# Kernel tuning notes

Measured on AMD Instinct MI355X. Metric: run time of the kernel, lower is better.

Reference implementation:

```python
import jax, jax.numpy as jnp
import numpy as np

TEMPERATURE = 0.1
SIGMA = 1.0
NUM_CLASSES = 4
INF = 1e8
EPS = 1e-12


def _l2_normalize(x):
    n = jnp.sqrt(jnp.sum(x * x, axis=-1, keepdims=True))
    return x / jnp.maximum(n, EPS)


def _rbf_kernel(y, gamma):
    # y: [M, P] -> [M, M] exp(-gamma * ||yi - yj||^2)
    sq = jnp.sum(y * y, axis=-1)
    d2 = sq[:, None] + sq[None, :] - 2.0 * (y @ y.T)
    d2 = jnp.maximum(d2, 0.0)
    return jnp.exp(-gamma * d2)


def setup_inputs() -> dict:
    key = jax.random.key(0)
    k1, k2, k3, k4 = jax.random.split(key, 4)
    N, D = 2048, 512
    return {
        "z_i": jax.random.normal(k1, (N, D), dtype=jnp.float32),
        "z_j": jax.random.normal(k2, (N, D), dtype=jnp.float32),
        "labels": jax.random.randint(k3, (N,), 0, NUM_CLASSES, dtype=jnp.int64),
        "z_pos": jax.random.uniform(k4, (N, 1), dtype=jnp.float32),
    }


def reference(z_i, z_j, labels, z_pos):
    N = z_i.shape[0]
    zi = _l2_normalize(z_i)
    zj = _l2_normalize(z_j)

    eye_n = jnp.eye(N, dtype=zi.dtype)
    sim_zii = (zi @ zi.T) / TEMPERATURE - INF * eye_n
    sim_zjj = (zj @ zj.T) / TEMPERATURE - INF * eye_n
    sim_zij = (zi @ zj.T) / TEMPERATURE

    # label agreement mask over the 2N x 2N augmented batch
    labs = jax.nn.one_hot(labels, NUM_CLASSES, dtype=jnp.float32)
    L = jnp.concatenate([labs, labs], axis=0)          # [2N, C]
    eye_2n = jnp.eye(2 * N, dtype=jnp.float32)
    mask = (L @ L.T) * (1.0 - eye_2n)

    # RBF kernel weights over positional labels (detached in original)
    all_pos = jnp.tile(z_pos.reshape(N, -1), (2, 1))   # [2N, P]
    gamma = 1.0 / (2.0 * SIGMA ** 2)
    weights = _rbf_kernel(all_pos, gamma) * (1.0 - eye_2n)

    final_weights = weights * mask
    # NB: torch broadcasting divides column j by rowsum[j]; matrix is symmetric
    final_weights = final_weights / final_weights.sum(axis=1)

    top = jnp.concatenate([sim_zii, sim_zij], axis=1)
    bot = jnp.concatenate([sim_zij.T, sim_zjj], axis=1)
    sim_Z = jnp.concatenate([top, bot], axis=0)        # [2N, 2N]

    log_sim_Z = jax.nn.log_softmax(sim_Z, axis=1)
    loss = (-1.0 / N) * jnp.sum(log_sim_Z * final_weights)
    return loss
```

## Files before the change

kernel.cpp:

```cpp
#include <hip/hip_runtime.h>
#include <hip/hip_bf16.h>

#define D 512
#define INV_T 10.0f
#define INF_VAL 1e8f

#define BM 128
#define BN 128
#define BK 64
#define KSTEPS (D / BK)
#define NCHUNK 64

typedef short bf16x8 __attribute__((ext_vector_type(8)));
typedef float f32x4 __attribute__((ext_vector_type(4)));

typedef __attribute__((address_space(3))) unsigned int lds_uint;
typedef __attribute__((address_space(1))) unsigned int gbl_uint;

__device__ __forceinline__ void async_copy16(const ushort* gsrc, ushort* ldst) {
  __builtin_amdgcn_global_load_lds((const gbl_uint*)gsrc, (lds_uint*)ldst, 16, 0, 0);
}

__device__ inline float wave_reduce_sum(float v) {
#pragma unroll
  for (int off = 32; off > 0; off >>= 1) v += __shfl_xor(v, off);
  return v;
}

__global__ __launch_bounds__(256) void k_normcast(const float* __restrict__ zi,
                                                  const float* __restrict__ zj,
                                                  ushort* __restrict__ zb, int N) {
  __shared__ float scratch[4];
  __shared__ float s_inv;
  int row = blockIdx.x;
  const float* src = (row < N) ? (zi + (size_t)row * D) : (zj + (size_t)(row - N) * D);
  float ss = 0.f;
  for (int k = threadIdx.x; k < D; k += 256) {
    float v = src[k];
    ss = fmaf(v, v, ss);
  }
  ss = wave_reduce_sum(ss);
  int lane = threadIdx.x & 63, wv = threadIdx.x >> 6;
  if (lane == 0) scratch[wv] = ss;
  __syncthreads();
  if (threadIdx.x == 0) {
    float t = scratch[0] + scratch[1] + scratch[2] + scratch[3];
    s_inv = 1.0f / fmaxf(sqrtf(t), 1e-12f);
  }
  __syncthreads();
  float sc = s_inv;
  ushort* dst = zb + (size_t)row * D;
  for (int k = threadIdx.x; k < D; k += 256) {
    __hip_bfloat16 h = __float2bfloat16(src[k] * sc);
    dst[k] = *reinterpret_cast<ushort*>(&h);
  }
}

__global__ __launch_bounds__(256) void k_colsum(const int* __restrict__ labels,
                                                const float* __restrict__ zpos,
                                                float* __restrict__ sinv, int N) {
  __shared__ float scratch[4];
  int j = blockIdx.x;
  int lj = labels[j];
  float pj = zpos[j];
  float s = 0.f;
  for (int i = threadIdx.x; i < N; i += 256) {
    if (labels[i] == lj) {
      float d = zpos[i] - pj;
      s += __expf(-0.5f * d * d);
    }
  }
  s = wave_reduce_sum(s);
  int lane = threadIdx.x & 63, wv = threadIdx.x >> 6;
  if (lane == 0) scratch[wv] = s;
  __syncthreads();
  if (threadIdx.x == 0) {
    float t = scratch[0] + scratch[1] + scratch[2] + scratch[3];
    sinv[j] = 1.0f / (2.0f * t - 1.0f);
  }
}

__global__ __launch_bounds__(256) void k_tt(const int* __restrict__ labels,
                                            const float* __restrict__ zpos,
                                            const float* __restrict__ sinv,
                                            float* __restrict__ tt, int N) {
  __shared__ float scratch[4];
  int i = blockIdx.x;
  int li = labels[i];
  float pi = zpos[i];
  float s = 0.f;
  for (int j = threadIdx.x; j < N; j += 256) {
    if (labels[j] == li) {
      float d = zpos[j] - pi;
      s += __expf(-0.5f * d * d) * sinv[j];
    }
  }
  s = wave_reduce_sum(s);
  int lane = threadIdx.x & 63, wv = threadIdx.x >> 6;
  if (lane == 0) scratch[wv] = s;
  __syncthreads();
  if (threadIdx.x == 0) {
    tt[i] = scratch[0] + scratch[1] + scratch[2] + scratch[3];
  }
}

__global__ __launch_bounds__(256, 4) void k_gemm(
    const ushort* __restrict__ zb, const int* __restrict__ labels,
    const float* __restrict__ zpos, const float* __restrict__ sinv,
    float* __restrict__ s_ws, float* __restrict__ c_ws, int N) {
  __shared__ __align__(16) ushort As[BM * BK];
  __shared__ __align__(16) ushort Bs[BN * BK];

  const int tid = threadIdx.x;
  const int lane = tid & 63;
  const int wv = tid >> 6;
  const int wr = wv >> 1;
  const int wc = wv & 1;
  const int colq = lane & 15;
  const int laneg = lane >> 4;

  const int bid = blockIdx.x;
  const int L = (bid & 7) * 128 + (bid >> 3);
  const int rt = L >> 5;
  const int ct = L & 31;
  const int rowBase = rt * BM;
  const int colBase = ct * BN;
  const int twoN = 2 * N;

  const int srow = lane >> 3;
  const int sslot = (lane & 7) ^ srow;

  f32x4 acc[4][4] = {};

  for (int kt = 0; kt < KSTEPS; ++kt) {
#pragma unroll
    for (int q = 0; q < 4; ++q) {
      int rloc = wv * 32 + q * 8;
      async_copy16(zb + (size_t)(rowBase + rloc + srow) * D + kt * BK + sslot * 8,
                   (ushort*)As + rloc * BK);
      async_copy16(zb + (size_t)(colBase + rloc + srow) * D + kt * BK + sslot * 8,
                   (ushort*)Bs + rloc * BK);
    }
    __syncthreads();

#pragma unroll
    for (int kk = 0; kk < 2; ++kk) {
      bf16x8 a[4], b[4];
      const int slot = (kk * 4 + laneg);
#pragma unroll
      for (int rf = 0; rf < 4; ++rf) {
        int r = wr * 64 + rf * 16 + colq;
        a[rf] = *reinterpret_cast<const bf16x8*>(
            reinterpret_cast<const char*>(As) + r * 128 + (slot ^ (r & 7)) * 16);
      }
#pragma unroll
      for (int cf = 0; cf < 4; ++cf) {
        int c = wc * 64 + cf * 16 + colq;
        b[cf] = *reinterpret_cast<const bf16x8*>(
            reinterpret_cast<const char*>(Bs) + c * 128 + (slot ^ (c & 7)) * 16);
      }
#pragma unroll
      for (int rf = 0; rf < 4; ++rf)
#pragma unroll
        for (int cf = 0; cf < 4; ++cf)
          acc[rf][cf] = __builtin_amdgcn_mfma_f32_16x16x32_bf16(a[rf], b[cf], acc[rf][cf], 0, 0, 0);
    }
    __syncthreads();
  }

  const int wRowBase = rowBase + wr * 64;
  const int wColBase = colBase + wc * 64;
  const int rmodBase = (wRowBase >= N) ? wRowBase - N : wRowBase;
  const int cmodBase = (wColBase >= N) ? wColBase - N : wColBase;

  float rpos[16];
  unsigned rlab = 0;
#pragma unroll
  for (int rf = 0; rf < 4; ++rf)
#pragma unroll
    for (int rg = 0; rg < 4; ++rg) {
      int idx = rf * 4 + rg;
      int r = rmodBase + rf * 16 + laneg * 4 + rg;
      rpos[idx] = zpos[r];
      rlab |= ((unsigned)labels[r] & 3u) << (idx * 2);
    }

  float s_p[16], c_p[16];
#pragma unroll
  for (int i = 0; i < 16; ++i) { s_p[i] = 0.f; c_p[i] = 0.f; }

#pragma unroll
  for (int cf = 0; cf < 4; ++cf) {
    int jc = cmodBase + cf * 16 + colq;
    int lc = labels[jc];
    float pc = zpos[jc];
    float si = sinv[jc];
    int col = wColBase + cf * 16 + colq;
#pragma unroll
    for (int rf = 0; rf < 4; ++rf)
#pragma unroll
      for (int rg = 0; rg < 4; ++rg) {
        int idx = rf * 4 + rg;
        int row = wRowBase + rf * 16 + laneg * 4 + rg;
        float sim = acc[rf][cf][rg] * INV_T;
        bool diag = (row == col);
        if (diag) sim = -INF_VAL;
        s_p[idx] += __expf(sim - 10.f);
        int lr = (int)((rlab >> (idx * 2)) & 3u);
        if (lr == lc && !diag) {
          float d = rpos[idx] - pc;
          c_p[idx] = fmaf(__expf(-0.5f * d * d) * si, sim, c_p[idx]);
        }
      }
  }

#pragma unroll
  for (int idx = 0; idx < 16; ++idx) {
#pragma unroll
    for (int off = 1; off < 16; off <<= 1) {
      s_p[idx] += __shfl_xor(s_p[idx], off);
      c_p[idx] += __shfl_xor(c_p[idx], off);
    }
  }
  if (colq == 0) {
    int cc = ct * 2 + wc;
#pragma unroll
    for (int rf = 0; rf < 4; ++rf)
#pragma unroll
      for (int rg = 0; rg < 4; ++rg) {
        int idx = rf * 4 + rg;
        int row = wRowBase + rf * 16 + laneg * 4 + rg;
        s_ws[(size_t)cc * twoN + row] = s_p[idx];
        c_ws[(size_t)cc * twoN + row] = c_p[idx];
      }
  }
}

__global__ __launch_bounds__(256) void k_combine(const float* __restrict__ s_ws,
                                                 const float* __restrict__ c_ws,
                                                 const float* __restrict__ sinv,
                                                 const float* __restrict__ tt,
                                                 float* __restrict__ partial, int N) {
  int a = blockIdx.x * 256 + threadIdx.x;
  int twoN = 2 * N;
  if (a >= twoN) return;
  float s = 0.f, c = 0.f;
  for (int cc = 0; cc < NCHUNK; ++cc) {
    s += s_ws[(size_t)cc * twoN + a];
    c += c_ws[(size_t)cc * twoN + a];
  }
  int ir = (a >= N) ? a - N : a;
  float lse = 10.f + logf(s);
  float wsum = 2.f * tt[ir] - sinv[ir];
  partial[a] = c - wsum * lse;
}

__global__ __launch_bounds__(256) void k_final(const float* __restrict__ partial,
                                               float* __restrict__ out, int N) {
  __shared__ float scratch[4];
  float s = 0.f;
  for (int a = threadIdx.x; a < 2 * N; a += 256) s += partial[a];
  s = wave_reduce_sum(s);
  int lane = threadIdx.x & 63, wv = threadIdx.x >> 6;
  if (lane == 0) scratch[wv] = s;
  __syncthreads();
  if (threadIdx.x == 0) {
    float t = scratch[0] + scratch[1] + scratch[2] + scratch[3];
    out[0] = (-1.0f / (float)N) * t;
  }
}

extern "C" void kernel_launch(void* const* d_in, const int* in_sizes, int n_in,
                              void* d_out, int out_size, void* d_ws, size_t ws_size,
                              hipStream_t stream) {
  (void)n_in; (void)out_size; (void)ws_size;
  const float* zi = (const float*)d_in[0];
  const float* zj = (const float*)d_in[1];
  const int* labels = (const int*)d_in[2];
  const float* zpos = (const float*)d_in[3];
  float* out = (float*)d_out;

  const int N = in_sizes[2];
  const int twoN = 2 * N;

  char* wsb = (char*)d_ws;
  ushort* zb = (ushort*)wsb;
  float* sinv = (float*)(wsb + (size_t)twoN * D * 2);
  float* tt = sinv + N;
  float* s_ws = tt + N;
  float* c_ws = s_ws + (size_t)NCHUNK * twoN;
  float* partial = c_ws + (size_t)NCHUNK * twoN;

  k_normcast<<<twoN, 256, 0, stream>>>(zi, zj, zb, N);
  k_colsum<<<N, 256, 0, stream>>>(labels, zpos, sinv, N);
  k_tt<<<N, 256, 0, stream>>>(labels, zpos, sinv, tt, N);
  k_gemm<<<(twoN / BM) * (twoN / BN), 256, 0, stream>>>(zb, labels, zpos, sinv, s_ws, c_ws, N);
  k_combine<<<(twoN + 255) / 256, 256, 0, stream>>>(s_ws, c_ws, sinv, tt, partial, N);
  k_final<<<1, 256, 0, stream>>>(partial, out, N);
}
```

Baseline: 70.39 us.

## Exploit symmetry with upper-triangular GEMM tiles, double-buffer loads, fuse prep kernels

The GEMM now launches only the upper-triangular tiles of the symmetric 2N×2N similarity matrix. Each off-diagonal tile also writes column-wise partial sums of the softmax denominators and weighted sims, standing in for the mirrored tile. K-loop loads are double-buffered in LDS so the next slice loads while MFMAs run, and diagonal tiles load only one operand. The normalize/cast and column-sum kernels are fused into one launch, with wave-per-row vectorized normalization. The costs are a serial loop to decode the tile index, larger LDS (occupancy hint lowered from 4 to 2), and extra shuffle reductions in the epilogue.

```diff
diff --git a/kernel.cpp b/kernel.cpp
--- a/kernel.cpp
+++ b/kernel.cpp
@@ -9,6 +9,8 @@
 #define BN 128
 #define BK 64
 #define KSTEPS (D / BK)
+#define NTB 32
+#define NBLK (NTB * (NTB + 1) / 2)
 #define NCHUNK 64
 
 typedef short bf16x8 __attribute__((ext_vector_type(8)));
@@ -27,56 +29,57 @@
   return v;
 }
 
-__global__ __launch_bounds__(256) void k_normcast(const float* __restrict__ zi,
-                                                  const float* __restrict__ zj,
-                                                  ushort* __restrict__ zb, int N) {
-  __shared__ float scratch[4];
-  __shared__ float s_inv;
-  int row = blockIdx.x;
-  const float* src = (row < N) ? (zi + (size_t)row * D) : (zj + (size_t)(row - N) * D);
-  float ss = 0.f;
-  for (int k = threadIdx.x; k < D; k += 256) {
-    float v = src[k];
-    ss = fmaf(v, v, ss);
-  }
-  ss = wave_reduce_sum(ss);
-  int lane = threadIdx.x & 63, wv = threadIdx.x >> 6;
-  if (lane == 0) scratch[wv] = ss;
-  __syncthreads();
-  if (threadIdx.x == 0) {
-    float t = scratch[0] + scratch[1] + scratch[2] + scratch[3];
-    s_inv = 1.0f / fmaxf(sqrtf(t), 1e-12f);
-  }
-  __syncthreads();
-  float sc = s_inv;
-  ushort* dst = zb + (size_t)row * D;
-  for (int k = threadIdx.x; k < D; k += 256) {
-    __hip_bfloat16 h = __float2bfloat16(src[k] * sc);
-    dst[k] = *reinterpret_cast<ushort*>(&h);
-  }
-}
-
-__global__ __launch_bounds__(256) void k_colsum(const int* __restrict__ labels,
-                                                const float* __restrict__ zpos,
-                                                float* __restrict__ sinv, int N) {
-  __shared__ float scratch[4];
-  int j = blockIdx.x;
-  int lj = labels[j];
-  float pj = zpos[j];
-  float s = 0.f;
-  for (int i = threadIdx.x; i < N; i += 256) {
-    if (labels[i] == lj) {
-      float d = zpos[i] - pj;
-      s += __expf(-0.5f * d * d);
-    }
-  }
-  s = wave_reduce_sum(s);
-  int lane = threadIdx.x & 63, wv = threadIdx.x >> 6;
-  if (lane == 0) scratch[wv] = s;
-  __syncthreads();
-  if (threadIdx.x == 0) {
-    float t = scratch[0] + scratch[1] + scratch[2] + scratch[3];
-    sinv[j] = 1.0f / (2.0f * t - 1.0f);
+__device__ __forceinline__ ushort f2bf(float x) {
+  __hip_bfloat16 h = __float2bfloat16(x);
+  return *reinterpret_cast<ushort*>(&h);
+}
+
+__global__ __launch_bounds__(256) void k_prep(const float* __restrict__ zi,
+                                              const float* __restrict__ zj,
+                                              ushort* __restrict__ zb,
+                                              const int* __restrict__ labels,
+                                              const float* __restrict__ zpos,
+                                              float* __restrict__ sinv, int N) {
+  int b = blockIdx.x;
+  if (b < 1024) {
+    int wv = threadIdx.x >> 6, lane = threadIdx.x & 63;
+    int row = b * 4 + wv;
+    const float* src = (row < N) ? (zi + (size_t)row * D) : (zj + (size_t)(row - N) * D);
+    const float4* s4 = reinterpret_cast<const float4*>(src);
+    float4 v0 = s4[lane];
+    float4 v1 = s4[lane + 64];
+    float ss = 0.f;
+    ss = fmaf(v0.x, v0.x, ss); ss = fmaf(v0.y, v0.y, ss);
+    ss = fmaf(v0.z, v0.z, ss); ss = fmaf(v0.w, v0.w, ss);
+    ss = fmaf(v1.x, v1.x, ss); ss = fmaf(v1.y, v1.y, ss);
+    ss = fmaf(v1.z, v1.z, ss); ss = fmaf(v1.w, v1.w, ss);
+    ss = wave_reduce_sum(ss);
+    float sc = 1.0f / fmaxf(sqrtf(ss), 1e-12f);
+    ushort4 o0 = {f2bf(v0.x * sc), f2bf(v0.y * sc), f2bf(v0.z * sc), f2bf(v0.w * sc)};
+    ushort4 o1 = {f2bf(v1.x * sc), f2bf(v1.y * sc), f2bf(v1.z * sc), f2bf(v1.w * sc)};
+    ushort4* dst = reinterpret_cast<ushort4*>(zb + (size_t)row * D);
+    dst[lane] = o0;
+    dst[lane + 64] = o1;
+  } else {
+    __shared__ float scratch[4];
+    int j = b - 1024;
+    int lj = labels[j];
+    float pj = zpos[j];
+    float s = 0.f;
+    for (int i = threadIdx.x; i < N; i += 256) {
+      if (labels[i] == lj) {
+        float d = zpos[i] - pj;
+        s += __expf(-0.5f * d * d);
+      }
+    }
+    s = wave_reduce_sum(s);
+    int lane = threadIdx.x & 63, wv = threadIdx.x >> 6;
+    if (lane == 0) scratch[wv] = s;
+    __syncthreads();
+    if (threadIdx.x == 0) {
+      float t = scratch[0] + scratch[1] + scratch[2] + scratch[3];
+      sinv[j] = 1.0f / (2.0f * t - 1.0f);
+    }
   }
 }
 
@@ -104,12 +107,11 @@
   }
 }
 
-__global__ __launch_bounds__(256, 4) void k_gemm(
+__global__ __launch_bounds__(256, 2) void k_gemm(
     const ushort* __restrict__ zb, const int* __restrict__ labels,
     const float* __restrict__ zpos, const float* __restrict__ sinv,
     float* __restrict__ s_ws, float* __restrict__ c_ws, int N) {
-  __shared__ __align__(16) ushort As[BM * BK];
-  __shared__ __align__(16) ushort Bs[BN * BK];
+  __shared__ __align__(16) ushort sT[2][2][BM * BK];
 
   const int tid = threadIdx.x;
   const int lane = tid & 63;
@@ -118,46 +120,65 @@
   const int wc = wv & 1;
   const int colq = lane & 15;
   const int laneg = lane >> 4;
+  const int twoN = 2 * N;
 
   const int bid = blockIdx.x;
-  const int L = (bid & 7) * 128 + (bid >> 3);
-  const int rt = L >> 5;
-  const int ct = L & 31;
+  int L = (bid & 7) * (NBLK / 8) + (bid >> 3);
+  int u = L, rt = 0;
+  while (u >= NTB - rt) { u -= NTB - rt; ++rt; }
+  const int ct = rt + u;
+  const bool diag = (rt == ct);
   const int rowBase = rt * BM;
   const int colBase = ct * BN;
-  const int twoN = 2 * N;
 
   const int srow = lane >> 3;
   const int sslot = (lane & 7) ^ srow;
 
   f32x4 acc[4][4] = {};
 
-  for (int kt = 0; kt < KSTEPS; ++kt) {
+  {
 #pragma unroll
     for (int q = 0; q < 4; ++q) {
       int rloc = wv * 32 + q * 8;
-      async_copy16(zb + (size_t)(rowBase + rloc + srow) * D + kt * BK + sslot * 8,
-                   (ushort*)As + rloc * BK);
-      async_copy16(zb + (size_t)(colBase + rloc + srow) * D + kt * BK + sslot * 8,
-                   (ushort*)Bs + rloc * BK);
-    }
-    __syncthreads();
-
+      async_copy16(zb + (size_t)(rowBase + rloc + srow) * D + 0 * BK + sslot * 8,
+                   (ushort*)sT[0][0] + rloc * BK);
+      if (!diag)
+        async_copy16(zb + (size_t)(colBase + rloc + srow) * D + 0 * BK + sslot * 8,
+                     (ushort*)sT[0][1] + rloc * BK);
+    }
+  }
+  __syncthreads();
+
+  int cur = 0;
+#pragma unroll
+  for (int kt = 0; kt < KSTEPS; ++kt) {
+    if (kt + 1 < KSTEPS) {
+#pragma unroll
+      for (int q = 0; q < 4; ++q) {
+        int rloc = wv * 32 + q * 8;
+        async_copy16(zb + (size_t)(rowBase + rloc + srow) * D + (kt + 1) * BK + sslot * 8,
+                     (ushort*)sT[cur ^ 1][0] + rloc * BK);
+        if (!diag)
+          async_copy16(zb + (size_t)(colBase + rloc + srow) * D + (kt + 1) * BK + sslot * 8,
+                       (ushort*)sT[cur ^ 1][1] + rloc * BK);
+      }
+    }
+
+    const char* Ab = reinterpret_cast<const char*>(sT[cur][0]);
+    const char* Bb = diag ? Ab : reinterpret_cast<const char*>(sT[cur][1]);
 #pragma unroll
     for (int kk = 0; kk < 2; ++kk) {
       bf16x8 a[4], b[4];
-      const int slot = (kk * 4 + laneg);
+      const int slot = kk * 4 + laneg;
 #pragma unroll
       for (int rf = 0; rf < 4; ++rf) {
         int r = wr * 64 + rf * 16 + colq;
-        a[rf] = *reinterpret_cast<const bf16x8*>(
-            reinterpret_cast<const char*>(As) + r * 128 + (slot ^ (r & 7)) * 16);
+        a[rf] = *reinterpret_cast<const bf16x8*>(Ab + r * 128 + (slot ^ (r & 7)) * 16);
       }
 #pragma unroll
       for (int cf = 0; cf < 4; ++cf) {
         int c = wc * 64 + cf * 16 + colq;
-        b[cf] = *reinterpret_cast<const bf16x8*>(
-            reinterpret_cast<const char*>(Bs) + c * 128 + (slot ^ (c & 7)) * 16);
+        b[cf] = *reinterpret_cast<const bf16x8*>(Bb + c * 128 + (slot ^ (c & 7)) * 16);
       }
 #pragma unroll
       for (int rf = 0; rf < 4; ++rf)
@@ -165,7 +186,11 @@
         for (int cf = 0; cf < 4; ++cf)
           acc[rf][cf] = __builtin_amdgcn_mfma_f32_16x16x32_bf16(a[rf], b[cf], acc[rf][cf], 0, 0, 0);
     }
-    __syncthreads();
+
+    if (kt + 1 < KSTEPS) {
+      __syncthreads();
+      cur ^= 1;
+    }
   }
 
   const int wRowBase = rowBase + wr * 64;
@@ -173,7 +198,7 @@
   const int rmodBase = (wRowBase >= N) ? wRowBase - N : wRowBase;
   const int cmodBase = (wColBase >= N) ? wColBase - N : wColBase;
 
-  float rpos[16];
+  float rpos[16], rsinv[16];
   unsigned rlab = 0;
 #pragma unroll
   for (int rf = 0; rf < 4; ++rf)
@@ -182,10 +207,11 @@
       int idx = rf * 4 + rg;
       int r = rmodBase + rf * 16 + laneg * 4 + rg;
       rpos[idx] = zpos[r];
+      rsinv[idx] = sinv[r];
       rlab |= ((unsigned)labels[r] & 3u) << (idx * 2);
     }
 
-  float s_p[16], c_p[16];
+  float s_p[16], c_p[16], sc_p[4], cc_p[4];
 #pragma unroll
   for (int i = 0; i < 16; ++i) { s_p[i] = 0.f; c_p[i] = 0.f; }
 
@@ -196,6 +222,7 @@
     float pc = zpos[jc];
     float si = sinv[jc];
     int col = wColBase + cf * 16 + colq;
+    float scf = 0.f, ccf = 0.f;
 #pragma unroll
     for (int rf = 0; rf < 4; ++rf)
 #pragma unroll
@@ -203,15 +230,21 @@
         int idx = rf * 4 + rg;
         int row = wRowBase + rf * 16 + laneg * 4 + rg;
         float sim = acc[rf][cf][rg] * INV_T;
-        bool diag = (row == col);
-        if (diag) sim = -INF_VAL;
-        s_p[idx] += __expf(sim - 10.f);
+        bool dg = (row == col);
+        if (dg) sim = -INF_VAL;
+        float e = __expf(sim - 10.f);
+        s_p[idx] += e;
+        scf += e;
         int lr = (int)((rlab >> (idx * 2)) & 3u);
-        if (lr == lc && !diag) {
+        if (lr == lc && !dg) {
           float d = rpos[idx] - pc;
-          c_p[idx] = fmaf(__expf(-0.5f * d * d) * si, sim, c_p[idx]);
+          float w = __expf(-0.5f * d * d);
+          c_p[idx] = fmaf(w * si, sim, c_p[idx]);
+          ccf = fmaf(w * rsinv[idx], sim, ccf);
         }
       }
+    sc_p[cf] = scf;
+    cc_p[cf] = ccf;
   }
 
 #pragma unroll
@@ -233,6 +266,25 @@
         s_ws[(size_t)cc * twoN + row] = s_p[idx];
         c_ws[(size_t)cc * twoN + row] = c_p[idx];
       }
+  }
+
+  if (!diag) {
+#pragma unroll
+    for (int cf = 0; cf < 4; ++cf) {
+      sc_p[cf] += __shfl_xor(sc_p[cf], 16);
+      sc_p[cf] += __shfl_xor(sc_p[cf], 32);
+      cc_p[cf] += __shfl_xor(cc_p[cf], 16);
+      cc_p[cf] += __shfl_xor(cc_p[cf], 32);
+    }
+    if (laneg == 0) {
+      int cct = rt * 2 + wr;
+#pragma unroll
+      for (int cf = 0; cf < 4; ++cf) {
+        int rowt = wColBase + cf * 16 + colq;
+        s_ws[(size_t)cct * twoN + rowt] = sc_p[cf];
+        c_ws[(size_t)cct * twoN + rowt] = cc_p[cf];
+      }
+    }
   }
 }
 
@@ -291,10 +343,9 @@
   float* c_ws = s_ws + (size_t)NCHUNK * twoN;
   float* partial = c_ws + (size_t)NCHUNK * twoN;
 
-  k_normcast<<<twoN, 256, 0, stream>>>(zi, zj, zb, N);
-  k_colsum<<<N, 256, 0, stream>>>(labels, zpos, sinv, N);
+  k_prep<<<1024 + 2048, 256, 0, stream>>>(zi, zj, zb, labels, zpos, sinv, N);
   k_tt<<<N, 256, 0, stream>>>(labels, zpos, sinv, tt, N);
-  k_gemm<<<(twoN / BM) * (twoN / BN), 256, 0, stream>>>(zb, labels, zpos, sinv, s_ws, c_ws, N);
+  k_gemm<<<NBLK, 256, 0, stream>>>(zb, labels, zpos, sinv, s_ws, c_ws, N);
   k_combine<<<(twoN + 255) / 256, 256, 0, stream>>>(s_ws, c_ws, sinv, tt, partial, N);
   k_final<<<1, 256, 0, stream>>>(partial, out, N);
 }
```

Measured after the change: 56.72 us. -19.4%, faster.
